# Optimization experiments

Hardware: AMD Instinct MI355X
Metric: run time of the kernel (lower is better)

The kernel has to match this reference:

```python
import jax, jax.numpy as jnp
import numpy as np

OUT_SIZE = 14
CUTOFF = 0.2
VAR0 = 4            # var[0], mixin_factor = 0.0 -> current std = var[0]
BETA = 4.0
N_SQ = OUT_SIZE * OUT_SIZE
TAU = 0.5 / N_SQ
BATCH = 256
CHANNELS = 512


def _gkern_np(kernlen, std, vmin, vmax):
    n = np.arange(kernlen) - (kernlen - 1) / 2.0
    w = np.exp(-(n ** 2) / (2.0 * std * std))
    g = np.outer(w, w)
    return g * (vmax - vmin) + vmin


def _build_templates():
    n = OUT_SIZE
    base = _gkern_np(2 * n - 1, VAR0, -CUTOFF, 1.0)
    base = np.maximum(base, 0.0) * 2.0 - 1.0
    base = TAU * np.clip(BETA * base / n, -1.0, None)  # clamp(min=-1) only
    # unfold(0,n,1).unfold(1,n,1).reshape(-1,n,n) == sliding windows, row-major
    t = np.lib.stride_tricks.sliding_window_view(base, (n, n)).reshape(-1, n, n)
    t = np.flip(t, axis=0).copy()  # torch.flip(templates, dims=(0,))
    templates_f = jnp.asarray(t, jnp.float32)                    # (n^2, n, n)
    neg = -TAU * jnp.ones((1, n, n), jnp.float32)
    templates_b = jnp.concatenate([templates_f, neg], axis=0)    # (n^2+1, n, n)
    alpha = N_SQ / (1.0 + N_SQ)
    p_T = jnp.asarray(
        np.array([alpha / N_SQ] * N_SQ + [1.0 - alpha], np.float32))  # (n^2+1,)
    return templates_f, templates_b, p_T


def setup_inputs() -> dict:
    key = jax.random.key(0)
    templates_f, templates_b, p_T = _build_templates()
    x = jax.random.normal(key, (BATCH, CHANNELS, OUT_SIZE, OUT_SIZE), jnp.float32)
    return {"x": x, "templates_f": templates_f,
            "templates_b": templates_b, "p_T": p_T}


def reference(x, templates_f, templates_b, p_T):
    B, C, H, W = x.shape
    tau = 0.5 / (H * W)
    # max_pool2d with kernel == full spatial extent -> flat argmax per (b, c)
    idx = jnp.argmax(x.reshape(B, C, H * W), axis=-1)            # (B, C) int
    sel = templates_f[idx]                                       # (B, C, H, W)
    mask = sel / jnp.max(sel)                                    # global max
    mask = jax.nn.relu(mask - CUTOFF) / CUTOFF
    x_masked = x * mask
    # local loss (mutual-information style) on the masked activations
    tr_x_T = jnp.einsum('bcwh,twh->cbt', x_masked * tau, templates_b)  # (C,B,T)
    p_x_T = jax.nn.softmax(tr_x_T, axis=1)                       # softmax over b
    p_x = jnp.einsum('t,cbt->cb', p_T, p_x_T)                    # (C, B)
    log_ratio = jnp.log(p_x_T / p_x[:, :, None])                 # (C, B, T)
    p_x_T_log = jnp.einsum('cbt,cbt->ct', p_x_T, log_ratio)      # (C, T)
    loss = -jnp.einsum('t,ct->c', p_T, p_x_T_log)                # (C,)
    return x_masked, mask, loss
```

## Files before the change

kernel.cpp:

```cpp
#include <hip/hip_runtime.h>

#define BB 256
#define CCH 512
#define HW 196
#define TT 197
#define TROWS 208
#define NFRAG (13 * 7)
#define ASHORTS (NFRAG * 64 * 8)

typedef __attribute__((ext_vector_type(8))) short bf16x8;
typedef __attribute__((ext_vector_type(4))) float f32x4;

__device__ __forceinline__ unsigned short f2bf(float f) {
    union { float f; unsigned u; } v; v.f = f;
    unsigned r = v.u + 0x7FFFu + ((v.u >> 16) & 1u);
    return (unsigned short)(r >> 16);
}

__global__ void prep(const float* __restrict__ tf, const float* __restrict__ tb,
                     float* __restrict__ wsf, unsigned short* __restrict__ tb_bf) {
    if (blockIdx.x < 182) {
        int i = blockIdx.x * 256 + threadIdx.x;
        int frag = i >> 9;
        int s    = i & 511;
        int mt = frag / 7, kt = frag % 7;
        int lane = s >> 3, j = s & 7;
        int r = mt * 16 + (lane & 15);
        int k = kt * 32 + (lane >> 4) * 8 + j;
        const float tau = 0.5f / 196.0f;
        float v = (r < TT && k < HW) ? tb[r * HW + k] * tau : 0.0f;
        tb_bf[i] = f2bf(v);
    } else {
        __shared__ float red[256];
        float m = -1e30f;
        for (int i = threadIdx.x; i < HW * HW; i += 256) m = fmaxf(m, tf[i]);
        red[threadIdx.x] = m;
        __syncthreads();
        for (int s = 128; s > 0; s >>= 1) {
            if (threadIdx.x < s) red[threadIdx.x] = fmaxf(red[threadIdx.x], red[threadIdx.x + s]);
            __syncthreads();
        }
        if (threadIdx.x == 0) wsf[0] = red[0];
    }
}

extern "C" __global__ __launch_bounds__(1024)
__attribute__((amdgpu_waves_per_eu(4, 4)))
void fused_one(const float* __restrict__ x, const float* __restrict__ tf,
               const float* __restrict__ pT, const unsigned short* __restrict__ tb_bf,
               const float* __restrict__ wsf,
               float* __restrict__ xm_out, float* __restrict__ mask_out,
               float* __restrict__ loss_out)
{
    extern __shared__ char smem[];
    unsigned short* Alds = (unsigned short*)smem;
    float* s_part = (float*)(smem + ASHORTS * 2);
    float* rAs    = s_part + 16 * TROWS;
    float* pTs    = rAs + TROWS;
    float* red    = pTs + TROWS;

    const int c    = blockIdx.x;
    const int tid  = threadIdx.x;
    const int lane = tid & 63;
    const int w    = tid >> 6;
    const int l15  = lane & 15, lg = lane >> 4;
    const float rg = 1.0f / wsf[0];

    {
        const f32x4* src = (const f32x4*)tb_bf;
        f32x4* dst = (f32x4*)Alds;
        #pragma unroll
        for (int it = 0; it < 6; ++it) {
            int idx = tid + it * 1024;
            if (idx < ASHORTS / 8) dst[idx] = src[idx];
        }
    }
    if (tid < TROWS) pTs[tid] = (tid < TT) ? pT[tid] : 0.0f;

    const int b = w * 16 + l15;
    const size_t rowoff = ((size_t)b * CCH + c) * HW;
    const float* xrow = x + rowoff;

    f32x4 u[13];
    #pragma unroll
    for (int kt = 0; kt < 6; ++kt) {
        u[2 * kt]     = *(const f32x4*)(xrow + kt * 32 + lg * 8);
        u[2 * kt + 1] = *(const f32x4*)(xrow + kt * 32 + lg * 8 + 4);
    }
    if (lg == 0) u[12] = *(const f32x4*)(xrow + 192);
    else         u[12] = (f32x4){-__builtin_inff(), -__builtin_inff(),
                                 -__builtin_inff(), -__builtin_inff()};

    float bv = -__builtin_inff(); int bi = 0;
    #pragma unroll
    for (int j = 0; j < 13; ++j) {
        const int k0 = (j < 12) ? (((j >> 1) * 8 + lg * 2 + (j & 1)) * 4) : 192;
        #pragma unroll
        for (int e = 0; e < 4; ++e) {
            float v = u[j][e];
            if (v > bv) { bv = v; bi = k0 + e; }
        }
    }
    #pragma unroll
    for (int m = 16; m <= 32; m <<= 1) {
        float ov = __shfl_xor(bv, m, 64);
        int   oi = __shfl_xor(bi, m, 64);
        if (ov > bv || (ov == bv && oi < bi)) { bv = ov; bi = oi; }
    }

    const float* selrow = tf + (size_t)bi * HW;
    float* xmrow = xm_out + rowoff;
    float* mkrow = mask_out + rowoff;
    bf16x8 fr[7];

    #pragma unroll
    for (int kt = 0; kt < 6; ++kt) {
        #pragma unroll
        for (int h = 0; h < 2; ++h) {
            const int k0 = kt * 32 + lg * 8 + h * 4;
            f32x4 sel = *(const f32x4*)(selrow + k0);
            f32x4 mk, xm;
            #pragma unroll
            for (int e = 0; e < 4; ++e) {
                float m = fmaxf(sel[e] * rg - 0.2f, 0.0f) * 5.0f;
                mk[e] = m;
                xm[e] = u[2 * kt + h][e] * m;
            }
            *(f32x4*)(xmrow + k0) = xm;
            *(f32x4*)(mkrow + k0) = mk;
            #pragma unroll
            for (int e = 0; e < 4; ++e) fr[kt][h * 4 + e] = (short)f2bf(xm[e]);
        }
    }
    {
        fr[6] = (bf16x8){0, 0, 0, 0, 0, 0, 0, 0};
        if (lg == 0) {
            f32x4 sel = *(const f32x4*)(selrow + 192);
            f32x4 mk, xm;
            #pragma unroll
            for (int e = 0; e < 4; ++e) {
                float m = fmaxf(sel[e] * rg - 0.2f, 0.0f) * 5.0f;
                mk[e] = m;
                xm[e] = u[12][e] * m;
            }
            *(f32x4*)(xmrow + 192) = xm;
            *(f32x4*)(mkrow + 192) = mk;
            #pragma unroll
            for (int e = 0; e < 4; ++e) fr[6][e] = (short)f2bf(xm[e]);
        }
    }

    __syncthreads();

    f32x4 acc[13];
    #pragma unroll
    for (int mt = 0; mt < 13; ++mt) acc[mt] = (f32x4){0.f, 0.f, 0.f, 0.f};

    const unsigned short* Abase = Alds + lane * 8;
    #pragma unroll
    for (int kt = 0; kt < 7; ++kt) {
        const bf16x8 bfrag = fr[kt];
        #pragma unroll
        for (int mt = 0; mt < 13; ++mt) {
            bf16x8 afrag = *(const bf16x8*)(Abase + (mt * 7 + kt) * 512);
            acc[mt] = __builtin_amdgcn_mfma_f32_16x16x32_bf16(afrag, bfrag, acc[mt], 0, 0, 0);
        }
    }

    float* sp = s_part + w * TROWS;
    #pragma unroll
    for (int mt = 0; mt < 13; ++mt) {
        #pragma unroll
        for (int e = 0; e < 4; ++e) acc[mt][e] = __expf(acc[mt][e]);
        f32x4 s = acc[mt];
        #pragma unroll
        for (int m = 1; m <= 8; m <<= 1) {
            #pragma unroll
            for (int e = 0; e < 4; ++e) s[e] += __shfl_xor(s[e], m, 64);
        }
        if (l15 == 0) *(f32x4*)(sp + mt * 16 + lg * 4) = s;
    }
    __syncthreads();
    if (tid < TROWS) {
        float s = 0.f;
        #pragma unroll
        for (int w2 = 0; w2 < 16; ++w2) s += s_part[w2 * TROWS + tid];
        rAs[tid] = 1.0f / s;
    }
    __syncthreads();

    float px = 0.f;
    #pragma unroll
    for (int mt = 0; mt < 13; ++mt) {
        const int t0 = mt * 16 + lg * 4;
        f32x4 ra = *(const f32x4*)(rAs + t0);
        f32x4 pt = *(const f32x4*)(pTs + t0);
        #pragma unroll
        for (int e = 0; e < 4; ++e) {
            float p = acc[mt][e] * ra[e];
            acc[mt][e] = p;
            px += pt[e] * p;
        }
    }
    px += __shfl_xor(px, 16, 64);
    px += __shfl_xor(px, 32, 64);
    const float rpx = 1.0f / px;

    float part = 0.f;
    #pragma unroll
    for (int mt = 0; mt < 13; ++mt) {
        const int t0 = mt * 16 + lg * 4;
        f32x4 pt = *(const f32x4*)(pTs + t0);
        #pragma unroll
        for (int e = 0; e < 4; ++e) {
            float p = acc[mt][e];
            part += pt[e] * p * __logf(p * rpx);
        }
    }
    #pragma unroll
    for (int off = 32; off >= 1; off >>= 1) part += __shfl_xor(part, off, 64);
    if (lane == 0) red[w] = part;
    __syncthreads();
    if (tid == 0) {
        float s = 0.f;
        #pragma unroll
        for (int w2 = 0; w2 < 16; ++w2) s += red[w2];
        loss_out[c] = -s;
    }
}

extern "C" void kernel_launch(void* const* d_in, const int* in_sizes, int n_in,
                              void* d_out, int out_size, void* d_ws, size_t ws_size,
                              hipStream_t stream) {
    const float* x  = (const float*)d_in[0];
    const float* tf = (const float*)d_in[1];
    const float* tb = (const float*)d_in[2];
    const float* pT = (const float*)d_in[3];

    const size_t NOUT = (size_t)BB * CCH * HW;
    float* xm_out = (float*)d_out;
    float* mk_out = xm_out + NOUT;
    float* ls_out = mk_out + NOUT;

    float* wsf = (float*)d_ws;
    unsigned short* tb_bf = (unsigned short*)((char*)d_ws + 64);

    prep<<<183, 256, 0, stream>>>(tf, tb, wsf, tb_bf);

    const size_t SMEM = (size_t)ASHORTS * 2
                      + 16 * TROWS * 4
                      + TROWS * 4 + TROWS * 4 + 16 * 4;
    hipFuncSetAttribute((const void*)fused_one, hipFuncAttributeMaxDynamicSharedMemorySize, (int)SMEM);
    fused_one<<<dim3(CCH), dim3(1024), SMEM, stream>>>(x, tf, pT, tb_bf, wsf,
                                                       xm_out, mk_out, ls_out);
}
```

Measured before the change: 146.1 us.

## Split fused kernel into streaming mask kernel and separate GEMM-loss kernel

Moves the argmax, mask and x_masked computation into a separate lightweight kernel, with four threads per row and fully coalesced loads and stores across many small blocks. The GEMM and loss kernel then reloads x_masked from global memory and converts it to bf16. This aims to give the bandwidth-heavy part better occupancy and memory parallelism than the 512 large blocks allowed. The cost is an extra full read of x_masked and one more kernel launch.

```diff
diff --git a/kernel.cpp b/kernel.cpp
--- a/kernel.cpp
+++ b/kernel.cpp
@@ -44,13 +44,66 @@
     }
 }
 
+extern "C" __global__ __launch_bounds__(256, 4)
+void k_stream(const float* __restrict__ x, const float* __restrict__ tf,
+              const float* __restrict__ wsf,
+              float* __restrict__ xm_out, float* __restrict__ mask_out)
+{
+    const int tid = threadIdx.x;
+    const int row = blockIdx.x * 64 + (tid >> 2);
+    const int q   = tid & 3;
+    const int nch = (q == 0) ? 13 : 12;
+    const float rg = 1.0f / wsf[0];
+
+    const size_t rowoff = (size_t)row * HW;
+    const float* xrow = x + rowoff;
+
+    f32x4 xv[13];
+    #pragma unroll
+    for (int j = 0; j < 13; ++j)
+        if (j < nch) xv[j] = *(const f32x4*)(xrow + (q + 4 * j) * 4);
+
+    float bv = -__builtin_inff(); int bi = 0;
+    #pragma unroll
+    for (int j = 0; j < 13; ++j) if (j < nch) {
+        const int k0 = (q + 4 * j) * 4;
+        #pragma unroll
+        for (int e = 0; e < 4; ++e) {
+            float v = xv[j][e];
+            if (v > bv) { bv = v; bi = k0 + e; }
+        }
+    }
+    #pragma unroll
+    for (int m = 1; m <= 2; m <<= 1) {
+        float ov = __shfl_xor(bv, m, 64);
+        int   oi = __shfl_xor(bi, m, 64);
+        if (ov > bv || (ov == bv && oi < bi)) { bv = ov; bi = oi; }
+    }
+
+    const float* selrow = tf + (size_t)bi * HW;
+    float* xmrow = xm_out + rowoff;
+    float* mkrow = mask_out + rowoff;
+
+    #pragma unroll
+    for (int j = 0; j < 13; ++j) if (j < nch) {
+        const int k0 = (q + 4 * j) * 4;
+        f32x4 sel = *(const f32x4*)(selrow + k0);
+        f32x4 mk, xm;
+        #pragma unroll
+        for (int e = 0; e < 4; ++e) {
+            float m = fmaxf(sel[e] * rg - 0.2f, 0.0f) * 5.0f;
+            mk[e] = m;
+            xm[e] = xv[j][e] * m;
+        }
+        *(f32x4*)(xmrow + k0) = xm;
+        *(f32x4*)(mkrow + k0) = mk;
+    }
+}
+
 extern "C" __global__ __launch_bounds__(1024)
-__attribute__((amdgpu_waves_per_eu(4, 4)))
-void fused_one(const float* __restrict__ x, const float* __restrict__ tf,
-               const float* __restrict__ pT, const unsigned short* __restrict__ tb_bf,
-               const float* __restrict__ wsf,
-               float* __restrict__ xm_out, float* __restrict__ mask_out,
-               float* __restrict__ loss_out)
+void k_gemm_loss(const float* __restrict__ xm, const float* __restrict__ pT,
+                 const unsigned short* __restrict__ tb_bf,
+                 float* __restrict__ loss_out)
 {
     extern __shared__ char smem[];
     unsigned short* Alds = (unsigned short*)smem;
@@ -64,7 +117,6 @@
     const int lane = tid & 63;
     const int w    = tid >> 6;
     const int l15  = lane & 15, lg = lane >> 4;
-    const float rg = 1.0f / wsf[0];
 
     {
         const f32x4* src = (const f32x4*)tb_bf;
@@ -78,76 +130,24 @@
     if (tid < TROWS) pTs[tid] = (tid < TT) ? pT[tid] : 0.0f;
 
     const int b = w * 16 + l15;
-    const size_t rowoff = ((size_t)b * CCH + c) * HW;
-    const float* xrow = x + rowoff;
-
-    f32x4 u[13];
+    const float* xrow = xm + ((size_t)b * CCH + c) * HW;
+
+    bf16x8 fr[7];
     #pragma unroll
     for (int kt = 0; kt < 6; ++kt) {
-        u[2 * kt]     = *(const f32x4*)(xrow + kt * 32 + lg * 8);
-        u[2 * kt + 1] = *(const f32x4*)(xrow + kt * 32 + lg * 8 + 4);
-    }
-    if (lg == 0) u[12] = *(const f32x4*)(xrow + 192);
-    else         u[12] = (f32x4){-__builtin_inff(), -__builtin_inff(),
-                                 -__builtin_inff(), -__builtin_inff()};
-
-    float bv = -__builtin_inff(); int bi = 0;
-    #pragma unroll
-    for (int j = 0; j < 13; ++j) {
-        const int k0 = (j < 12) ? (((j >> 1) * 8 + lg * 2 + (j & 1)) * 4) : 192;
-        #pragma unroll
-        for (int e = 0; e < 4; ++e) {
-            float v = u[j][e];
-            if (v > bv) { bv = v; bi = k0 + e; }
-        }
-    }
-    #pragma unroll
-    for (int m = 16; m <= 32; m <<= 1) {
-        float ov = __shfl_xor(bv, m, 64);
-        int   oi = __shfl_xor(bi, m, 64);
-        if (ov > bv || (ov == bv && oi < bi)) { bv = ov; bi = oi; }
-    }
-
-    const float* selrow = tf + (size_t)bi * HW;
-    float* xmrow = xm_out + rowoff;
-    float* mkrow = mask_out + rowoff;
-    bf16x8 fr[7];
-
-    #pragma unroll
-    for (int kt = 0; kt < 6; ++kt) {
-        #pragma unroll
-        for (int h = 0; h < 2; ++h) {
-            const int k0 = kt * 32 + lg * 8 + h * 4;
-            f32x4 sel = *(const f32x4*)(selrow + k0);
-            f32x4 mk, xm;
-            #pragma unroll
-            for (int e = 0; e < 4; ++e) {
-                float m = fmaxf(sel[e] * rg - 0.2f, 0.0f) * 5.0f;
-                mk[e] = m;
-                xm[e] = u[2 * kt + h][e] * m;
-            }
-            *(f32x4*)(xmrow + k0) = xm;
-            *(f32x4*)(mkrow + k0) = mk;
-            #pragma unroll
-            for (int e = 0; e < 4; ++e) fr[kt][h * 4 + e] = (short)f2bf(xm[e]);
-        }
-    }
-    {
-        fr[6] = (bf16x8){0, 0, 0, 0, 0, 0, 0, 0};
-        if (lg == 0) {
-            f32x4 sel = *(const f32x4*)(selrow + 192);
-            f32x4 mk, xm;
-            #pragma unroll
-            for (int e = 0; e < 4; ++e) {
-                float m = fmaxf(sel[e] * rg - 0.2f, 0.0f) * 5.0f;
-                mk[e] = m;
-                xm[e] = u[12][e] * m;
-            }
-            *(f32x4*)(xmrow + 192) = xm;
-            *(f32x4*)(mkrow + 192) = mk;
-            #pragma unroll
-            for (int e = 0; e < 4; ++e) fr[6][e] = (short)f2bf(xm[e]);
-        }
+        f32x4 u0 = *(const f32x4*)(xrow + kt * 32 + lg * 8);
+        f32x4 u1 = *(const f32x4*)(xrow + kt * 32 + lg * 8 + 4);
+        #pragma unroll
+        for (int e = 0; e < 4; ++e) {
+            fr[kt][e]     = (short)f2bf(u0[e]);
+            fr[kt][e + 4] = (short)f2bf(u1[e]);
+        }
+    }
+    fr[6] = (bf16x8){0, 0, 0, 0, 0, 0, 0, 0};
+    if (lg == 0) {
+        f32x4 u0 = *(const f32x4*)(xrow + 192);
+        #pragma unroll
+        for (int e = 0; e < 4; ++e) fr[6][e] = (short)f2bf(u0[e]);
     }
 
     __syncthreads();
@@ -246,11 +246,11 @@
     unsigned short* tb_bf = (unsigned short*)((char*)d_ws + 64);
 
     prep<<<183, 256, 0, stream>>>(tf, tb, wsf, tb_bf);
+    k_stream<<<2048, 256, 0, stream>>>(x, tf, wsf, xm_out, mk_out);
 
     const size_t SMEM = (size_t)ASHORTS * 2
                       + 16 * TROWS * 4
                       + TROWS * 4 + TROWS * 4 + 16 * 4;
-    hipFuncSetAttribute((const void*)fused_one, hipFuncAttributeMaxDynamicSharedMemorySize, (int)SMEM);
-    fused_one<<<dim3(CCH), dim3(1024), SMEM, stream>>>(x, tf, pT, tb_bf, wsf,
-                                                       xm_out, mk_out, ls_out);
-}
+    hipFuncSetAttribute((const void*)k_gemm_loss, hipFuncAttributeMaxDynamicSharedMemorySize, (int)SMEM);
+    k_gemm_loss<<<dim3(CCH), dim3(1024), SMEM, stream>>>(xm_out, pT, tb_bf, ls_out);
+}
```

Result: slower. 158.8 us (+8.6%).

## Split template LDS staging into two halves to shrink shared memory footprint

Applied to the files above, without the earlier changes.

The bf16 template matrix is no longer staged into LDS all at once. It is loaded in two chunks: 7 M-tiles first, then the remaining 6 after a barrier, reusing the same buffer. This cuts dynamic LDS per block roughly in half, aiming to let more workgroups reside on a CU. The fixed waves_per_eu hint is also dropped. The cost is an extra pair of barriers and a serialized second LDS fill between the two MFMA phases, and occupancy may still be capped by register use.

```diff
diff --git a/kernel.cpp b/kernel.cpp
--- a/kernel.cpp
+++ b/kernel.cpp
@@ -7,6 +7,10 @@
 #define TROWS 208
 #define NFRAG (13 * 7)
 #define ASHORTS (NFRAG * 64 * 8)
+#define H1FRAG (7 * 7)
+#define H2FRAG (6 * 7)
+#define H1SHORTS (H1FRAG * 512)
+#define H2SHORTS (H2FRAG * 512)
 
 typedef __attribute__((ext_vector_type(8))) short bf16x8;
 typedef __attribute__((ext_vector_type(4))) float f32x4;
@@ -45,7 +49,6 @@
 }
 
 extern "C" __global__ __launch_bounds__(1024)
-__attribute__((amdgpu_waves_per_eu(4, 4)))
 void fused_one(const float* __restrict__ x, const float* __restrict__ tf,
                const float* __restrict__ pT, const unsigned short* __restrict__ tb_bf,
                const float* __restrict__ wsf,
@@ -54,7 +57,7 @@
 {
     extern __shared__ char smem[];
     unsigned short* Alds = (unsigned short*)smem;
-    float* s_part = (float*)(smem + ASHORTS * 2);
+    float* s_part = (float*)(smem + H1SHORTS * 2);
     float* rAs    = s_part + 16 * TROWS;
     float* pTs    = rAs + TROWS;
     float* red    = pTs + TROWS;
@@ -70,9 +73,9 @@
         const f32x4* src = (const f32x4*)tb_bf;
         f32x4* dst = (f32x4*)Alds;
         #pragma unroll
-        for (int it = 0; it < 6; ++it) {
+        for (int it = 0; it < 4; ++it) {
             int idx = tid + it * 1024;
-            if (idx < ASHORTS / 8) dst[idx] = src[idx];
+            if (idx < H1SHORTS / 8) dst[idx] = src[idx];
         }
     }
     if (tid < TROWS) pTs[tid] = (tid < TT) ? pT[tid] : 0.0f;
@@ -161,8 +164,31 @@
     for (int kt = 0; kt < 7; ++kt) {
         const bf16x8 bfrag = fr[kt];
         #pragma unroll
-        for (int mt = 0; mt < 13; ++mt) {
+        for (int mt = 0; mt < 7; ++mt) {
             bf16x8 afrag = *(const bf16x8*)(Abase + (mt * 7 + kt) * 512);
+            acc[mt] = __builtin_amdgcn_mfma_f32_16x16x32_bf16(afrag, bfrag, acc[mt], 0, 0, 0);
+        }
+    }
+
+    __syncthreads();
+
+    {
+        const f32x4* src = (const f32x4*)(tb_bf + H1SHORTS);
+        f32x4* dst = (f32x4*)Alds;
+        #pragma unroll
+        for (int it = 0; it < 3; ++it) {
+            int idx = tid + it * 1024;
+            if (idx < H2SHORTS / 8) dst[idx] = src[idx];
+        }
+    }
+    __syncthreads();
+
+    #pragma unroll
+    for (int kt = 0; kt < 7; ++kt) {
+        const bf16x8 bfrag = fr[kt];
+        #pragma unroll
+        for (int mt = 7; mt < 13; ++mt) {
+            bf16x8 afrag = *(const bf16x8*)(Abase + ((mt - 7) * 7 + kt) * 512);
             acc[mt] = __builtin_amdgcn_mfma_f32_16x16x32_bf16(afrag, bfrag, acc[mt], 0, 0, 0);
         }
     }
@@ -247,7 +273,7 @@
 
     prep<<<183, 256, 0, stream>>>(tf, tb, wsf, tb_bf);
 
-    const size_t SMEM = (size_t)ASHORTS * 2
+    const size_t SMEM = (size_t)H1SHORTS * 2
                       + 16 * TROWS * 4
                       + TROWS * 4 + TROWS * 4 + 16 * 4;
     hipFuncSetAttribute((const void*)fused_one, hipFuncAttributeMaxDynamicSharedMemorySize, (int)SMEM);
```

Result: no change. 144.2 us (-1.3%).
